# Optimization experiments

Hardware: AMD Instinct MI355X
Metric: run time of the kernel (lower is better)

Reference implementation:

```python
import jax, jax.numpy as jnp
import numpy as np

NBITS = 8
MAXQ = float(2**NBITS - 1)  # 255 for uint8 asymmetric quantization


def asym_quantize(x):
    """Per-tensor asymmetric quantization to the [0, 255] grid.

    x ~ scale * (q - zero), with scale = (max-min)/255, zero = round(-min/scale).
    Returns (q, scale, zero) with q kept in float32 holding integer values.
    """
    xmax = jnp.max(x)
    xmin = jnp.min(x)
    scale = (xmax - xmin) / MAXQ
    zero = jnp.round(-xmin / scale)
    q = jnp.clip(jnp.round(x / scale) + zero, 0.0, MAXQ)
    return q, scale, zero


def setup_inputs() -> dict:
    key = jax.random.key(0)
    kA, kB = jax.random.split(key)
    A = jax.random.normal(kA, (4096, 2048), dtype=jnp.float32)
    B = jax.random.normal(kB, (2048, 4096), dtype=jnp.float32)
    return {"A": A, "B": B}


def reference(A, B):
    # Quantize both operands per-tensor asymmetrically.
    qA, sA, zA = asym_quantize(A)  # [M, K]
    qB, sB, zB = asym_quantize(B)  # [K, N]
    K = A.shape[1]

    # Integer GEMM on the quantized values (exact int accumulation in int32).
    acc = jnp.matmul(qA.astype(jnp.int32), qB.astype(jnp.int32)).astype(jnp.float32)  # [M, N]

    # Fused asymmetric dequant epilogue:
    # A @ B = sA*sB * (qA@qB - zA * colsum(qB) - zB * rowsum(qA) + K*zA*zB)
    rowsum_qA = jnp.sum(qA, axis=1, keepdims=True)   # [M, 1]
    colsum_qB = jnp.sum(qB, axis=0, keepdims=True)   # [1, N]
    out = (sA * sB) * (acc - zA * colsum_qB - zB * rowsum_qA
                       + jnp.float32(K) * zA * zB)
    return out
```

## Files before the change

### kernel.cpp

```cpp
#include <hip/hip_runtime.h>
#include <math.h>


#define M_DIM 4096
#define K_DIM 2048
#define N_DIM 4096

using int4v = __attribute__((ext_vector_type(4))) int;
using int16v = __attribute__((ext_vector_type(16))) int;

typedef __attribute__((address_space(1))) const void glb_cv;
typedef __attribute__((address_space(3))) void lds_v;

__device__ __forceinline__ int qbyte(float x, float rs, float z) {
    float q = fminf(fmaxf(rintf(x * rs) + z, 0.0f), 255.0f);
    return (int)q - 128;
}

__device__ __forceinline__ int sum4(int w) {
    return (int)(signed char)(w) + (int)(signed char)(w >> 8) +
           (int)(signed char)(w >> 16) + (int)(signed char)(w >> 24);
}

__global__ void minmax_stage1(const float* __restrict__ A,
                              const float* __restrict__ B,
                              float* __restrict__ partials,
                              int* __restrict__ colB) {
    int b = blockIdx.x;
    if (b < 16) colB[b * 256 + threadIdx.x] = 0;
    const float* src = (b < 512) ? A : B;
    int lb = (b < 512) ? b : b - 512;
    const float4* v = (const float4*)src + (long)lb * 4096;
    float mn = INFINITY, mx = -INFINITY;
    for (int i = threadIdx.x; i < 4096; i += 256) {
        float4 x = v[i];
        mn = fminf(mn, fminf(fminf(x.x, x.y), fminf(x.z, x.w)));
        mx = fmaxf(mx, fmaxf(fmaxf(x.x, x.y), fmaxf(x.z, x.w)));
    }
    for (int off = 32; off; off >>= 1) {
        mn = fminf(mn, __shfl_down(mn, off));
        mx = fmaxf(mx, __shfl_down(mx, off));
    }
    __shared__ float smn[4], smx[4];
    int w = threadIdx.x >> 6;
    if ((threadIdx.x & 63) == 0) { smn[w] = mn; smx[w] = mx; }
    __syncthreads();
    if (threadIdx.x == 0) {
        mn = fminf(fminf(smn[0], smn[1]), fminf(smn[2], smn[3]));
        mx = fmaxf(fmaxf(smx[0], smx[1]), fmaxf(smx[2], smx[3]));
        partials[2 * b] = mn;
        partials[2 * b + 1] = mx;
    }
}

__global__ void quant_fused(const float* __restrict__ A,
                            const float* __restrict__ B,
                            const float* __restrict__ partials,
                            signed char* __restrict__ A8,
                            signed char* __restrict__ B8T,
                            int* __restrict__ rowA,
                            int* __restrict__ colB,
                            float* __restrict__ qp) {
    int b = blockIdx.x, t = threadIdx.x;

    float mnA = INFINITY, mxA = -INFINITY, mnB = INFINITY, mxB = -INFINITY;
    for (int i = t; i < 512; i += 256) {
        mnA = fminf(mnA, partials[2 * i]);
        mxA = fmaxf(mxA, partials[2 * i + 1]);
        mnB = fminf(mnB, partials[2 * (i + 512)]);
        mxB = fmaxf(mxB, partials[2 * (i + 512) + 1]);
    }
    for (int off = 32; off; off >>= 1) {
        mnA = fminf(mnA, __shfl_down(mnA, off));
        mxA = fmaxf(mxA, __shfl_down(mxA, off));
        mnB = fminf(mnB, __shfl_down(mnB, off));
        mxB = fmaxf(mxB, __shfl_down(mxB, off));
    }
    __shared__ float sred[4][4];
    int w = t >> 6;
    if ((t & 63) == 0) { sred[w][0] = mnA; sred[w][1] = mxA; sred[w][2] = mnB; sred[w][3] = mxB; }
    __syncthreads();
    mnA = fminf(fminf(sred[0][0], sred[1][0]), fminf(sred[2][0], sred[3][0]));
    mxA = fmaxf(fmaxf(sred[0][1], sred[1][1]), fmaxf(sred[2][1], sred[3][1]));
    mnB = fminf(fminf(sred[0][2], sred[1][2]), fminf(sred[2][2], sred[3][2]));
    mxB = fmaxf(fmaxf(sred[0][3], sred[1][3]), fmaxf(sred[2][3], sred[3][3]));
    float sA = (mxA - mnA) / 255.0f;
    float zA = rintf(-mnA / sA);
    float sB = (mxB - mnB) / 255.0f;
    float zB = rintf(-mnB / sB);
    if (b == 0 && t == 0) { qp[0] = sA; qp[1] = zA; qp[2] = sB; qp[3] = zB; }
    __syncthreads();

    if (b < 2048) {
        float rs = 1.0f / sA, z = zA;
        long base = (long)b * 4096 + (long)t * 16;
        const float4* v = (const float4*)(A + base);
        union { signed char c[16]; int4 i4; } u;
        int ls = 0;
#pragma unroll
        for (int j = 0; j < 4; j++) {
            float4 x = v[j];
            int q0 = qbyte(x.x, rs, z), q1 = qbyte(x.y, rs, z);
            int q2 = qbyte(x.z, rs, z), q3 = qbyte(x.w, rs, z);
            u.c[j * 4 + 0] = (signed char)q0;
            u.c[j * 4 + 1] = (signed char)q1;
            u.c[j * 4 + 2] = (signed char)q2;
            u.c[j * 4 + 3] = (signed char)q3;
            ls += q0 + q1 + q2 + q3;
        }
        *(int4*)(A8 + base) = u.i4;
        for (int off = 32; off; off >>= 1) ls += __shfl_down(ls, off);
        __shared__ int wsum[4];
        if ((t & 63) == 0) wsum[t >> 6] = ls;
        __syncthreads();
        if (t == 0) rowA[b * 2] = wsum[0] + wsum[1];
        if (t == 128) rowA[b * 2 + 1] = wsum[2] + wsum[3];
    } else {
        float rs = 1.0f / sB, z = zB;
        int bb = b - 2048;
        int k0 = (bb & 31) * 64, n0 = (bb >> 5) * 64;
        __shared__ int tile[64][17];
        int cn = (t & 15) * 4;
        int kg = (t >> 4) * 4;
        int w0 = 0, w1 = 0, w2 = 0, w3 = 0;
#pragma unroll
        for (int r = 0; r < 4; r++) {
            float4 x = *(const float4*)&B[(long)(k0 + kg + r) * N_DIM + n0 + cn];
            w0 |= (qbyte(x.x, rs, z) & 255) << (8 * r);
            w1 |= (qbyte(x.y, rs, z) & 255) << (8 * r);
            w2 |= (qbyte(x.z, rs, z) & 255) << (8 * r);
            w3 |= (qbyte(x.w, rs, z) & 255) << (8 * r);
        }
        int kc = kg >> 2;
        tile[cn + 0][kc] = w0;
        tile[cn + 1][kc] = w1;
        tile[cn + 2][kc] = w2;
        tile[cn + 3][kc] = w3;
        __syncthreads();
        int n2 = t >> 2, kb = (t & 3) * 4;
        int4 v;
        v.x = tile[n2][kb + 0];
        v.y = tile[n2][kb + 1];
        v.z = tile[n2][kb + 2];
        v.w = tile[n2][kb + 3];
        *(int4*)&B8T[(long)(n0 + n2) * K_DIM + k0 + (t & 3) * 16] = v;
        int ls = sum4(v.x) + sum4(v.y) + sum4(v.z) + sum4(v.w);
        ls += __shfl_down(ls, 2);
        ls += __shfl_down(ls, 1);
        if ((t & 3) == 0) atomicAdd(&colB[n0 + n2], ls);
    }
}

__global__ __launch_bounds__(256, 3) void gemm_i8(
        const signed char* __restrict__ A8,
        const signed char* __restrict__ B8T,
        const int* __restrict__ rowA,
        const int* __restrict__ colB,
        const float* __restrict__ qp,
        float* __restrict__ out) {
    __shared__ __align__(16) signed char As[128 * 128];
    __shared__ __align__(16) signed char Bs[128 * 128];

    int b = blockIdx.x;
    int xcd = b & 7, i0 = b >> 3;
    int reg = xcd + 8 * (i0 >> 6);
    int jj0 = i0 & 63;
    int mt = (reg >> 2) * 8 + (jj0 >> 3);
    int nt = (reg & 3) * 8 + (jj0 & 7);
    int r0 = mt * 128, c0 = nt * 128;

    int t = threadIdx.x, lane = t & 63, wave = t >> 6;
    int l31 = lane & 31;
    int lh = lane >> 5;
    int wm = (wave >> 1) * 64;
    int wn = (wave & 1) * 64;

    int16v acc[2][2];
#pragma unroll
    for (int i = 0; i < 2; i++)
#pragma unroll
        for (int j = 0; j < 2; j++)
#pragma unroll
            for (int r = 0; r < 16; r++) acc[i][j][r] = 0;

    long aoff[4], boff[4];
#pragma unroll
    for (int j = 0; j < 4; j++) {
        int ch = t + 256 * j;
        int row = ch >> 3, p = ch & 7;
        int gk = p ^ (row & 7);
        aoff[j] = (long)(r0 + row) * K_DIM + gk * 16;
        boff[j] = (long)(c0 + row) * K_DIM + gk * 16;
    }

    int arow0 = wm + l31, arow1 = wm + 32 + l31;
    int brow0 = wn + l31, brow1 = wn + 32 + l31;

    for (int k0 = 0; k0 < K_DIM; k0 += 128) {
        __syncthreads();
#pragma unroll
        for (int j = 0; j < 4; j++)
            __builtin_amdgcn_global_load_lds((glb_cv*)(A8 + aoff[j] + k0),
                                             (lds_v*)(As + (t + 256 * j) * 16), 16, 0, 0);
#pragma unroll
        for (int j = 0; j < 4; j++)
            __builtin_amdgcn_global_load_lds((glb_cv*)(B8T + boff[j] + k0),
                                             (lds_v*)(Bs + (t + 256 * j) * 16), 16, 0, 0);
        __syncthreads();

#pragma unroll
        for (int ks = 0; ks < 4; ks++) {
            int c = ks * 2 + lh;
            int4v af0 = *(const int4v*)&As[arow0 * 128 + ((c ^ (arow0 & 7)) * 16)];
            int4v af1 = *(const int4v*)&As[arow1 * 128 + ((c ^ (arow1 & 7)) * 16)];
            int4v bf0 = *(const int4v*)&Bs[brow0 * 128 + ((c ^ (brow0 & 7)) * 16)];
            int4v bf1 = *(const int4v*)&Bs[brow1 * 128 + ((c ^ (brow1 & 7)) * 16)];
            acc[0][0] = __builtin_amdgcn_mfma_i32_32x32x32_i8(af0, bf0, acc[0][0], 0, 0, 0);
            acc[0][1] = __builtin_amdgcn_mfma_i32_32x32x32_i8(af0, bf1, acc[0][1], 0, 0, 0);
            acc[1][0] = __builtin_amdgcn_mfma_i32_32x32x32_i8(af1, bf0, acc[1][0], 0, 0, 0);
            acc[1][1] = __builtin_amdgcn_mfma_i32_32x32x32_i8(af1, bf1, acc[1][1], 0, 0, 0);
        }
    }

    float sA = qp[0], zA = qp[1], sB = qp[2], zB = qp[3];
    int cA = 128 - (int)zA, cB = 128 - (int)zB;
    float ss = sA * sB;
    int Kzz = K_DIM * cA * cB;
#pragma unroll
    for (int fm = 0; fm < 2; fm++) {
        int rbase = r0 + wm + fm * 32 + 4 * lh;
        int ra[16];
#pragma unroll
        for (int rq = 0; rq < 4; rq++) {
            int4 rv = *(const int4*)&rowA[rbase + 8 * rq];
            ra[rq * 4 + 0] = cB * rv.x + Kzz;
            ra[rq * 4 + 1] = cB * rv.y + Kzz;
            ra[rq * 4 + 2] = cB * rv.z + Kzz;
            ra[rq * 4 + 3] = cB * rv.w + Kzz;
        }
#pragma unroll
        for (int fn = 0; fn < 2; fn++) {
            int cc = c0 + wn + fn * 32 + l31;
            int can = cA * colB[cc];
#pragma unroll
            for (int r = 0; r < 16; r++) {
                int row = rbase + (r & 3) + 8 * (r >> 2);
                int v = acc[fm][fn][r] + ra[(r >> 2) * 4 + (r & 3)] + can;
                __builtin_nontemporal_store(ss * (float)v, &out[(long)row * N_DIM + cc]);
            }
        }
    }
}

extern "C" void kernel_launch(void* const* d_in, const int* in_sizes, int n_in,
                              void* d_out, int out_size, void* d_ws, size_t ws_size,
                              hipStream_t stream) {
    const float* A = (const float*)d_in[0];
    const float* B = (const float*)d_in[1];
    float* out = (float*)d_out;
    char* ws = (char*)d_ws;

    signed char* A8  = (signed char*)ws;
    signed char* B8T = (signed char*)(ws + 8388608);
    int*   rowA      = (int*)(ws + 16777216);
    int*   colB      = (int*)(ws + 16793600);
    float* partials  = (float*)(ws + 16809984);
    float* qp        = (float*)(ws + 16818176);

    minmax_stage1<<<1024, 256, 0, stream>>>(A, B, partials, colB);
    quant_fused<<<4096, 256, 0, stream>>>(A, B, partials, A8, B8T, rowA, colB, qp);
    gemm_i8<<<1024, 256, 0, stream>>>(A8, B8T, rowA, colB, qp, out);
}
```

Baseline: 164.4 us.

## Switch int8 GEMM to 16x16x64 MFMA tiles with 4x4 fragments per wave

Replaces the 32x32x32 i8 MFMA inner loop with 16x16x64 i8 MFMA, giving each wave a 4x4 grid of 16x16 accumulators and loading fragments with the matching 16-row/4-group lane mapping. The epilogue is rewritten for the new accumulator layout. Launch bounds are also raised from 3 to 4 blocks per CU to push occupancy. The intent is to improve MFMA throughput and fragment reuse. The risk is higher register pressure or spilling under the tighter launch bound.

```diff
diff --git a/kernel.cpp b/kernel.cpp
--- a/kernel.cpp
+++ b/kernel.cpp
@@ -7,7 +7,6 @@
 #define N_DIM 4096
 
 using int4v = __attribute__((ext_vector_type(4))) int;
-using int16v = __attribute__((ext_vector_type(16))) int;
 
 typedef __attribute__((address_space(1))) const void glb_cv;
 typedef __attribute__((address_space(3))) void lds_v;
@@ -151,7 +150,7 @@
     }
 }
 
-__global__ __launch_bounds__(256, 3) void gemm_i8(
+__global__ __launch_bounds__(256, 4) void gemm_i8(
         const signed char* __restrict__ A8,
         const signed char* __restrict__ B8T,
         const int* __restrict__ rowA,
@@ -170,55 +169,57 @@
     int r0 = mt * 128, c0 = nt * 128;
 
     int t = threadIdx.x, lane = t & 63, wave = t >> 6;
-    int l31 = lane & 31;
-    int lh = lane >> 5;
+    int mrow = lane & 15;
+    int g = lane >> 4;
     int wm = (wave >> 1) * 64;
     int wn = (wave & 1) * 64;
 
-    int16v acc[2][2];
-#pragma unroll
-    for (int i = 0; i < 2; i++)
-#pragma unroll
-        for (int j = 0; j < 2; j++)
-#pragma unroll
-            for (int r = 0; r < 16; r++) acc[i][j][r] = 0;
+    int4v acc[4][4];
+#pragma unroll
+    for (int i = 0; i < 4; i++)
+#pragma unroll
+        for (int jj = 0; jj < 4; jj++) acc[i][jj] = (int4v){0, 0, 0, 0};
 
     long aoff[4], boff[4];
 #pragma unroll
-    for (int j = 0; j < 4; j++) {
-        int ch = t + 256 * j;
+    for (int jj = 0; jj < 4; jj++) {
+        int ch = t + 256 * jj;
         int row = ch >> 3, p = ch & 7;
         int gk = p ^ (row & 7);
-        aoff[j] = (long)(r0 + row) * K_DIM + gk * 16;
-        boff[j] = (long)(c0 + row) * K_DIM + gk * 16;
-    }
-
-    int arow0 = wm + l31, arow1 = wm + 32 + l31;
-    int brow0 = wn + l31, brow1 = wn + 32 + l31;
+        aoff[jj] = (long)(r0 + row) * K_DIM + gk * 16;
+        boff[jj] = (long)(c0 + row) * K_DIM + gk * 16;
+    }
+
+    int swz = (mrow & 7);
 
     for (int k0 = 0; k0 < K_DIM; k0 += 128) {
         __syncthreads();
 #pragma unroll
-        for (int j = 0; j < 4; j++)
-            __builtin_amdgcn_global_load_lds((glb_cv*)(A8 + aoff[j] + k0),
-                                             (lds_v*)(As + (t + 256 * j) * 16), 16, 0, 0);
-#pragma unroll
-        for (int j = 0; j < 4; j++)
-            __builtin_amdgcn_global_load_lds((glb_cv*)(B8T + boff[j] + k0),
-                                             (lds_v*)(Bs + (t + 256 * j) * 16), 16, 0, 0);
-        __syncthreads();
-
-#pragma unroll
-        for (int ks = 0; ks < 4; ks++) {
-            int c = ks * 2 + lh;
-            int4v af0 = *(const int4v*)&As[arow0 * 128 + ((c ^ (arow0 & 7)) * 16)];
-            int4v af1 = *(const int4v*)&As[arow1 * 128 + ((c ^ (arow1 & 7)) * 16)];
-            int4v bf0 = *(const int4v*)&Bs[brow0 * 128 + ((c ^ (brow0 & 7)) * 16)];
-            int4v bf1 = *(const int4v*)&Bs[brow1 * 128 + ((c ^ (brow1 & 7)) * 16)];
-            acc[0][0] = __builtin_amdgcn_mfma_i32_32x32x32_i8(af0, bf0, acc[0][0], 0, 0, 0);
-            acc[0][1] = __builtin_amdgcn_mfma_i32_32x32x32_i8(af0, bf1, acc[0][1], 0, 0, 0);
-            acc[1][0] = __builtin_amdgcn_mfma_i32_32x32x32_i8(af1, bf0, acc[1][0], 0, 0, 0);
-            acc[1][1] = __builtin_amdgcn_mfma_i32_32x32x32_i8(af1, bf1, acc[1][1], 0, 0, 0);
+        for (int jj = 0; jj < 4; jj++)
+            __builtin_amdgcn_global_load_lds((glb_cv*)(A8 + aoff[jj] + k0),
+                                             (lds_v*)(As + (t + 256 * jj) * 16), 16, 0, 0);
+#pragma unroll
+        for (int jj = 0; jj < 4; jj++)
+            __builtin_amdgcn_global_load_lds((glb_cv*)(B8T + boff[jj] + k0),
+                                             (lds_v*)(Bs + (t + 256 * jj) * 16), 16, 0, 0);
+        __syncthreads();
+
+#pragma unroll
+        for (int ks = 0; ks < 2; ks++) {
+            int c = ks * 4 + g;
+            int koff = (c ^ swz) * 16;
+            int4v af[4], bf[4];
+#pragma unroll
+            for (int i = 0; i < 4; i++)
+                af[i] = *(const int4v*)&As[(wm + i * 16 + mrow) * 128 + koff];
+#pragma unroll
+            for (int jj = 0; jj < 4; jj++)
+                bf[jj] = *(const int4v*)&Bs[(wn + jj * 16 + mrow) * 128 + koff];
+#pragma unroll
+            for (int i = 0; i < 4; i++)
+#pragma unroll
+                for (int jj = 0; jj < 4; jj++)
+                    acc[i][jj] = __builtin_amdgcn_mfma_i32_16x16x64_i8(af[i], bf[jj], acc[i][jj], 0, 0, 0);
         }
     }
 
@@ -226,27 +227,22 @@
     int cA = 128 - (int)zA, cB = 128 - (int)zB;
     float ss = sA * sB;
     int Kzz = K_DIM * cA * cB;
-#pragma unroll
-    for (int fm = 0; fm < 2; fm++) {
-        int rbase = r0 + wm + fm * 32 + 4 * lh;
-        int ra[16];
-#pragma unroll
-        for (int rq = 0; rq < 4; rq++) {
-            int4 rv = *(const int4*)&rowA[rbase + 8 * rq];
-            ra[rq * 4 + 0] = cB * rv.x + Kzz;
-            ra[rq * 4 + 1] = cB * rv.y + Kzz;
-            ra[rq * 4 + 2] = cB * rv.z + Kzz;
-            ra[rq * 4 + 3] = cB * rv.w + Kzz;
-        }
-#pragma unroll
-        for (int fn = 0; fn < 2; fn++) {
-            int cc = c0 + wn + fn * 32 + l31;
+    int ocol = c0 + wn + mrow;
+    int orow = r0 + wm + g * 4;
+#pragma unroll
+    for (int i = 0; i < 4; i++) {
+        int ra[4];
+#pragma unroll
+        for (int rr = 0; rr < 4; rr++) ra[rr] = cB * rowA[orow + i * 16 + rr] + Kzz;
+#pragma unroll
+        for (int jj = 0; jj < 4; jj++) {
+            int cc = ocol + jj * 16;
             int can = cA * colB[cc];
 #pragma unroll
-            for (int r = 0; r < 16; r++) {
-                int row = rbase + (r & 3) + 8 * (r >> 2);
-                int v = acc[fm][fn][r] + ra[(r >> 2) * 4 + (r & 3)] + can;
-                __builtin_nontemporal_store(ss * (float)v, &out[(long)row * N_DIM + cc]);
+            for (int rr = 0; rr < 4; rr++) {
+                int v = acc[i][jj][rr] + ra[rr] + can;
+                __builtin_nontemporal_store(ss * (float)v,
+                                            &out[(long)(orow + i * 16 + rr) * N_DIM + cc]);
             }
         }
     }
```

Result: no change. 162.1 us (-1.4%).
